# Optimization experiments

Hardware: AMD Instinct MI355X
Metric: run time of the kernel (lower is better)

Reference implementation:

```python
import jax, jax.numpy as jnp
import numpy as np


def _pick(key, nodes, mask, cnt):
    # Uniformly pick one of the `cnt` entries of `nodes` where mask is True.
    r = jax.random.randint(key, (), 0, jnp.maximum(cnt, 1))
    cs = jnp.cumsum(mask.astype(jnp.int32))
    return nodes[jnp.argmax(cs == r + 1)]


def _one_walk(key, nbrs, f0, n_faces, L):
    # nbrs: [N,3] int32 neighbor table, f0: scalar start face.
    seq = jnp.zeros((L + 1,), jnp.int32).at[0].set(f0)
    visited = jnp.zeros((n_faces + 1,), bool).at[n_faces].set(True).at[f0].set(True)

    def cond(st):
        return st[2] <= L

    def body(st):
        seq, visited, i, bs, k = st
        k, k1, k2, k3 = jax.random.split(k, 4)
        cur = seq[i - 1]
        nb = nbrs[cur]                     # [3] neighbor candidates
        unv = ~visited[nb]
        cnt = unv.sum()
        need = cnt == 0                    # stuck -> backtrack
        cand = _pick(k1, nb, unv, cnt)

        def bcond(c):
            bs_c, found = c[0], c[1]
            return need & (~found) & (i > bs_c)

        def bbody(c):
            bs_c, found, ta, kk = c
            kk, kp = jax.random.split(kk)
            back = seq[i - bs_c - 1]
            bn = nbrs[back]
            bm = ~visited[bn]
            bc = bm.sum()
            f2 = bc > 0
            ta2 = _pick(kp, bn, bm, bc)
            return (jnp.where(f2, bs_c, bs_c + 2), f2, jnp.where(f2, ta2, ta), kk)

        bs_f, found, ta_bt, _ = jax.lax.while_loop(
            bcond, bbody, (bs, jnp.array(False), jnp.int32(0), k2))
        rand_node = jax.random.randint(k3, (), 0, n_faces, dtype=jnp.int32)
        to_add = jnp.where(~need, cand, jnp.where(found, ta_bt, rand_node))
        hit = need & found                 # successful backtrack
        bs_new = jnp.where(hit, bs_f, jnp.int32(1))
        i_new = jnp.where(hit, i - bs_f, i)
        ar = jnp.arange(L + 1, dtype=jnp.int32)
        # torch: replace seq[i-bs:i] with to_add on successful backtrack
        seq = jnp.where(hit & (ar >= i_new) & (ar < i), to_add, seq)
        visited = visited.at[to_add].set(True)
        seq = seq.at[i_new].set(to_add)
        return (seq, visited, i_new + 1, bs_new, k)

    seq, *_ = jax.lax.while_loop(
        cond, body, (seq, visited, jnp.int32(1), jnp.int32(1), key))
    return seq


def patch_random_walk(key, neighbors, centers, n_faces, seq_len):
    B, G = centers.shape
    keys = jax.random.split(key, B * G).reshape(B, G)
    walk_g = jax.vmap(_one_walk, in_axes=(0, None, 0, None, None))
    walk_bg = jax.vmap(walk_g, in_axes=(0, 0, 0, None, None))
    return walk_bg(keys, neighbors, centers, n_faces, seq_len)  # [B,G,L+1] int32


def setup_inputs() -> dict:
    key = jax.random.key(0)
    k1, k2, k3 = jax.random.split(key, 3)
    B, N, G = 4, 20000, 1024
    xyz = jax.random.normal(k1, (B, N, 3), dtype=jnp.float32)
    neighbors = jax.random.randint(k2, (B, N, 3), 0, N, dtype=jnp.int32)
    centers = jax.random.randint(k3, (B, G), 0, N, dtype=jnp.int32)
    return {"xyz": xyz, "neighbors": neighbors, "centers": centers,
            "n_faces": N, "seq_len": 63}


def reference(xyz, neighbors, centers, n_faces, seq_len):
    # patch_random_walk -> idx [B,G,K]; then Group.forward gather + recenter.
    idx = patch_random_walk(jax.random.key(42), neighbors, centers, n_faces, seq_len)
    gather = jax.vmap(lambda p, i: p[i])(xyz, idx)            # [B,G,K,3]
    center_xyz = jax.vmap(lambda p, c: p[c])(xyz, centers)    # [B,G,3]
    return gather - center_xyz[:, :, None, :]
```

## Files before the change

kernel.cpp:

```cpp
#include <hip/hip_runtime.h>
#include <stdint.h>
#include <stddef.h>


namespace {

__device__ __forceinline__ uint32_t rotl32(uint32_t x, int r) {
  return (x << r) | (x >> (32 - r));
}

__device__ __forceinline__ void tf2x32(uint32_t ka, uint32_t kb,
                                       uint32_t x0, uint32_t x1,
                                       uint32_t& o0, uint32_t& o1) {
  const uint32_t kc = ka ^ kb ^ 0x1BD11BDAu;
  x0 += ka; x1 += kb;
#define TF_R4(r0, r1, r2, r3)                          \
  x0 += x1; x1 = rotl32(x1, r0); x1 ^= x0;             \
  x0 += x1; x1 = rotl32(x1, r1); x1 ^= x0;             \
  x0 += x1; x1 = rotl32(x1, r2); x1 ^= x0;             \
  x0 += x1; x1 = rotl32(x1, r3); x1 ^= x0;
  TF_R4(13, 15, 26, 6)  x0 += kb; x1 += kc + 1u;
  TF_R4(17, 29, 16, 24) x0 += kc; x1 += ka + 2u;
  TF_R4(13, 15, 26, 6)  x0 += ka; x1 += kb + 3u;
  TF_R4(17, 29, 16, 24) x0 += kb; x1 += kc + 4u;
  TF_R4(13, 15, 26, 6)  x0 += kc; x1 += ka + 5u;
#undef TF_R4
  o0 = x0; o1 = x1;
}

__device__ __forceinline__ void randbits(uint32_t ka, uint32_t kb,
                                         uint32_t& hi, uint32_t& lo) {
  uint32_t s0a, s0b, s1a, s1b, h0, h1;
  tf2x32(ka, kb, 0u, 0u, s0a, s0b);
  tf2x32(ka, kb, 0u, 1u, s1a, s1b);
  tf2x32(s0a, s0b, 0u, 0u, h0, h1);
  hi = h0 ^ h1;
  tf2x32(s1a, s1b, 0u, 0u, h0, h1);
  lo = h0 ^ h1;
}

__device__ __forceinline__ uint32_t r_generic(uint32_t hi, uint32_t lo,
                                              uint32_t span) {
  uint32_t mult = 65536u % span;
  mult = (mult * mult) % span;
  return ((hi % span) * mult + (lo % span)) % span;
}

__device__ __forceinline__ uint32_t pick_code(uint32_t hi, uint32_t lo) {
  return ((hi % 3u + lo % 3u) % 3u) | ((lo & 1u) << 2);
}

constexpr int WPB = 16;
constexpr int CH = 64;
constexpr int NMAX = 20352;
constexpr int VISW = 636;

__global__ __launch_bounds__(1024) void walk_kernel(
    const float* __restrict__ xyz, const int* __restrict__ nbrs,
    const int* __restrict__ centers, const int* __restrict__ n_faces_p,
    const int* __restrict__ seq_len_p, float* __restrict__ out,
    int s0, int num_walks, int Lp1) {
  __shared__ uint32_t nb01L[NMAX];
  __shared__ uint16_t nb2L[NMAX];
  __shared__ uint32_t visL[WPB * VISW];

  const int tid = threadIdx.x;
  const int wv = tid >> 6, lane = tid & 63;
  const int w0 = blockIdx.x * WPB;
  if (w0 >= num_walks) return;
  const int w = w0 + wv;
  const bool active = (w < num_walks);

  const int N = *n_faces_p;
  const int L = *seq_len_p;
  const int B = s0 / (3 * N);
  const int G = num_walks / B;
  const bool lds_ok = (N <= NMAX) && (G % WPB == 0);

  const int bb = (active ? w : w0) / G;
  const int* __restrict__ nb   = nbrs + (size_t)bb * N * 3;
  const float* __restrict__ xb = xyz + (size_t)bb * N * 3;

  const int f0 = active ? centers[w] : 0;
  int3 grow = make_int3(0, 0, 0);
  if (!lds_ok && active)
    grow = *reinterpret_cast<const int3*>(nb + 3 * (size_t)f0);

  if (wv == 0) {
    if (lane < WPB && (w0 + lane) < num_walks) {
      uint32_t ka, kb;
      tf2x32(0u, 42u, 0u, (uint32_t)(w0 + lane), ka, kb);
      visL[(lane * CH + 0) * 2 + 0] = ka;
      visL[(lane * CH + 0) * 2 + 1] = kb;
#pragma clang loop unroll(disable)
      for (int c2 = 1; c2 < CH; ++c2) {
        tf2x32(ka, kb, 0u, 0u, ka, kb);
        visL[(lane * CH + c2) * 2 + 0] = ka;
        visL[(lane * CH + c2) * 2 + 1] = kb;
      }
    }
  } else if (lds_ok) {
    for (int r = tid - 64; r < N; r += 960) {
      const int3 v = *reinterpret_cast<const int3*>(nb + 3 * (size_t)r);
      nb01L[r] = (uint32_t)v.x | ((uint32_t)v.y << 16);
      nb2L[r]  = (uint16_t)v.z;
    }
  }
  __syncthreads();

  const uint32_t mka = visL[(wv * CH + lane) * 2 + 0];
  const uint32_t mkb = visL[(wv * CH + lane) * 2 + 1];
  uint32_t mycode;
  {
    uint32_t k1a, k1b, hi, lo;
    tf2x32(mka, mkb, 0u, 1u, k1a, k1b);
    randbits(k1a, k1b, hi, lo);
    mycode = pick_code(hi, lo);
  }
  __syncthreads();

  if (!active) return;

  uint32_t extka = 0, extkb = 0;
  int extc = -1;
  auto get_key = [&](int idx, uint32_t& ra, uint32_t& rb) {
    if (idx < CH) {
      ra = (uint32_t)__shfl((int)mka, idx);
      rb = (uint32_t)__shfl((int)mkb, idx);
    } else {
      if (extc < 0) {
        extka = (uint32_t)__shfl((int)mka, CH - 1);
        extkb = (uint32_t)__shfl((int)mkb, CH - 1);
        extc = CH - 1;
      }
      while (extc < idx) { tf2x32(extka, extkb, 0u, 0u, extka, extkb); ++extc; }
      ra = extka; rb = extkb;
    }
  };

  int seqr = (lane == 0) ? f0 : -1;
  uint32_t code_next = (uint32_t)__shfl((int)mycode, 0);
  int i = 1, bs = 1, c = 0;

  if (lds_ok) {
    uint32_t* __restrict__ visW = visL + wv * VISW;
    for (int j = lane; j < VISW; j += 64) visW[j] = 0u;
    if (lane == 0) visW[(unsigned)f0 >> 5] = 1u << (f0 & 31);

    uint32_t p0 = nb01L[f0];
    int n0 = (int)(p0 & 0xffffu), n1 = (int)(p0 >> 16), n2 = (int)nb2L[f0];

    while (i <= L) {
      const int idx = c; ++c;
      const uint32_t pA = nb01L[n0]; const uint32_t a2 = nb2L[n0];
      const uint32_t pB = nb01L[n1]; const uint32_t b2 = nb2L[n1];
      const uint32_t pC = nb01L[n2]; const uint32_t c2v = nb2L[n2];
      const uint32_t wv0 = visW[(unsigned)n0 >> 5];
      const uint32_t wv1 = visW[(unsigned)n1 >> 5];
      const uint32_t wv2 = visW[(unsigned)n2 >> 5];
      const uint32_t codeP = code_next;
      code_next = (uint32_t)__shfl((int)mycode, (c < CH) ? c : 0);

      const uint32_t u0 = ((wv0 >> (n0 & 31)) & 1u) ^ 1u;
      const uint32_t u1 = ((wv1 >> (n1 & 31)) & 1u) ^ 1u;
      const uint32_t u2 = ((wv2 >> (n2 & 31)) & 1u) ^ 1u;
      const uint32_t cnt = u0 + u1 + u2;

      int to_add, sel;
      if (__builtin_expect(cnt == 0, 0)) {
        sel = -1;
        uint32_t kia, kib;
        get_key(idx, kia, kib);
        uint32_t kka, kkb;
        tf2x32(kia, kib, 0u, 2u, kka, kkb);
        bool found = false;
        int ta = 0, bsc = bs;
        while (!found && i > bsc) {
          uint32_t ca, cb, kpa, kpb;
          tf2x32(kka, kkb, 0u, 0u, ca, cb);
          tf2x32(kka, kkb, 0u, 1u, kpa, kpb);
          const int back = __shfl(seqr, i - bsc - 1);
          const uint32_t pm = nb01L[back];
          const int m0 = (int)(pm & 0xffffu), m1 = (int)(pm >> 16);
          const int m2 = (int)nb2L[back];
          const uint32_t e0 = ((visW[(unsigned)m0 >> 5] >> (m0 & 31)) & 1u) ^ 1u;
          const uint32_t e1 = ((visW[(unsigned)m1 >> 5] >> (m1 & 31)) & 1u) ^ 1u;
          const uint32_t e2 = ((visW[(unsigned)m2 >> 5] >> (m2 & 31)) & 1u) ^ 1u;
          const uint32_t bc = e0 + e1 + e2;
          if (bc > 0) {
            uint32_t bhi, blo;
            randbits(kpa, kpb, bhi, blo);
            const uint32_t bcode = pick_code(bhi, blo);
            const uint32_t r3 = bcode & 3u, r2 = (bcode >> 2) & 1u;
            const uint32_t t2v = (bc == 3 ? r3 : (bc == 2 ? r2 : 0)) + 1;
            ta = (e0 == t2v) ? m0 : ((e0 + e1 == t2v) ? m1 : m2);
            found = true;
          } else {
            bsc += 2;
          }
          kka = ca; kkb = cb;
        }
        if (found) {
          to_add = ta;
          const int i_new = i - bsc;
          seqr = (lane >= i_new && lane < i) ? to_add : seqr;
          bs = bsc; i = i_new;
        } else {
          uint32_t k3a, k3b, rhi, rlo;
          tf2x32(kia, kib, 0u, 3u, k3a, k3b);
          randbits(k3a, k3b, rhi, rlo);
          to_add = (int)r_generic(rhi, rlo, (uint32_t)N);
          bs = 1;
        }
        if (lane == 0)
          visW[(unsigned)to_add >> 5] |= 1u << (to_add & 31);
        seqr = (lane == i) ? to_add : seqr;
        ++i;
        const uint32_t p = nb01L[to_add];
        n0 = (int)(p & 0xffffu); n1 = (int)(p >> 16); n2 = (int)nb2L[to_add];
        continue;
      }
      uint32_t code = codeP;
      if (__builtin_expect(idx >= CH, 0)) {
        uint32_t ia, ib, k1a, k1b, hi, lo;
        get_key(idx, ia, ib);
        tf2x32(ia, ib, 0u, 1u, k1a, k1b);
        randbits(k1a, k1b, hi, lo);
        code = pick_code(hi, lo);
      }
      const uint32_t r3 = code & 3u, r2 = (code >> 2) & 1u;
      const uint32_t target = (cnt == 3 ? r3 : (cnt == 2 ? r2 : 0)) + 1;
      sel = (u0 == target) ? 0 : ((u0 + u1 == target) ? 1 : 2);
      to_add = (sel == 0) ? n0 : ((sel == 1) ? n1 : n2);
      const uint32_t wsel = (sel == 0) ? wv0 : ((sel == 1) ? wv1 : wv2);
      if (lane == 0)
        visW[(unsigned)to_add >> 5] = wsel | (1u << (to_add & 31));
      seqr = (lane == i) ? to_add : seqr;
      bs = 1; ++i;
      if (sel == 0)      { n0 = (int)(pA & 0xffffu); n1 = (int)(pA >> 16); n2 = (int)a2; }
      else if (sel == 1) { n0 = (int)(pB & 0xffffu); n1 = (int)(pB >> 16); n2 = (int)b2; }
      else               { n0 = (int)(pC & 0xffffu); n1 = (int)(pC >> 16); n2 = (int)c2v; }
    }
  } else {
    int hist  = (lane == 0) ? f0 : -1;
    int hist2 = -1;
    int3 row = grow;
    while (i <= L) {
      const int idx = c; ++c;
      const bool deep = (idx >= CH);
      const uint32_t codeP = code_next;
      code_next = (uint32_t)__shfl((int)mycode, (c < CH) ? c : 0);

      const int n0 = row.x, n1 = row.y, n2 = row.z;
      int v0 = __any(hist == n0), v1 = __any(hist == n1), v2 = __any(hist == n2);
      if (deep) {
        v0 |= __any(hist2 == n0); v1 |= __any(hist2 == n1); v2 |= __any(hist2 == n2);
      }
      const int u0 = 1 - v0, u1 = 1 - v1, u2 = 1 - v2;
      const int cnt = u0 + u1 + u2;

      int to_add;
      bool hit = false;
      int bsf = bs;
      if (cnt > 0) {
        uint32_t code = codeP;
        if (deep) {
          uint32_t ia, ib, k1a, k1b, hi, lo;
          get_key(idx, ia, ib);
          tf2x32(ia, ib, 0u, 1u, k1a, k1b);
          randbits(k1a, k1b, hi, lo);
          code = pick_code(hi, lo);
        }
        const int r3 = (int)(code & 3u), r2 = (int)((code >> 2) & 1u);
        const int target = (cnt == 3 ? r3 : (cnt == 2 ? r2 : 0)) + 1;
        to_add = (u0 == target) ? n0 : ((u0 + u1 == target) ? n1 : n2);
      } else {
        uint32_t kia, kib;
        get_key(idx, kia, kib);
        uint32_t kka, kkb;
        tf2x32(kia, kib, 0u, 2u, kka, kkb);
        bool found = false;
        int ta = 0, bsc = bs;
        while (!found && i > bsc) {
          uint32_t ca, cb, kpa, kpb;
          tf2x32(kka, kkb, 0u, 0u, ca, cb);
          tf2x32(kka, kkb, 0u, 1u, kpa, kpb);
          const int back = __shfl(seqr, i - bsc - 1);
          const int3 br = *reinterpret_cast<const int3*>(nb + 3 * (size_t)back);
          int w0m = __any(hist == br.x), w1m = __any(hist == br.y), w2m = __any(hist == br.z);
          if (deep) {
            w0m |= __any(hist2 == br.x); w1m |= __any(hist2 == br.y); w2m |= __any(hist2 == br.z);
          }
          const int e0 = 1 - w0m, e1 = 1 - w1m, e2 = 1 - w2m;
          const int bc = e0 + e1 + e2;
          if (bc > 0) {
            uint32_t bhi, blo;
            randbits(kpa, kpb, bhi, blo);
            const uint32_t bcode = pick_code(bhi, blo);
            const int r3 = (int)(bcode & 3u), r2 = (int)((bcode >> 2) & 1u);
            const int t2v = (bc == 3 ? r3 : (bc == 2 ? r2 : 0)) + 1;
            ta = (e0 == t2v) ? br.x : ((e0 + e1 == t2v) ? br.y : br.z);
            found = true;
          } else {
            bsc += 2;
          }
          kka = ca; kkb = cb;
        }
        if (found) {
          to_add = ta; hit = true; bsf = bsc;
        } else {
          uint32_t k3a, k3b, rhi, rlo;
          tf2x32(kia, kib, 0u, 3u, k3a, k3b);
          randbits(k3a, k3b, rhi, rlo);
          to_add = (int)r_generic(rhi, rlo, (uint32_t)N);
        }
      }

      int i_new, up;
      if (hit) { i_new = i - bsf; bs = bsf; up = i - 1; }
      else     { i_new = i;       bs = 1;   up = i; }
      seqr = (lane >= i_new && lane <= up) ? to_add : seqr;

      const int slot = idx + 1;
      if (slot < CH)          hist  = (lane == slot)      ? to_add : hist;
      else if (slot < 2 * CH) hist2 = (lane == slot - CH) ? to_add : hist2;

      i = i_new + 1;
      row = *reinterpret_cast<const int3*>(nb + 3 * (size_t)to_add);
    }
  }

  const float cx = xb[3 * (size_t)f0 + 0];
  const float cy = xb[3 * (size_t)f0 + 1];
  const float cz = xb[3 * (size_t)f0 + 2];
  if (lane < Lp1) {
    const int node = seqr;
    float3 v;
    v.x = xb[3 * (size_t)node + 0] - cx;
    v.y = xb[3 * (size_t)node + 1] - cy;
    v.z = xb[3 * (size_t)node + 2] - cz;
    *reinterpret_cast<float3*>(out + ((size_t)w * Lp1 + lane) * 3) = v;
  }
}

}

extern "C" void kernel_launch(void* const* d_in, const int* in_sizes, int n_in,
                              void* d_out, int out_size, void* d_ws, size_t ws_size,
                              hipStream_t stream) {
  const float* xyz     = (const float*)d_in[0];
  const int*   nbrs    = (const int*)d_in[1];
  const int*   centers = (const int*)d_in[2];
  const int*   n_faces = (const int*)d_in[3];
  const int*   seq_len = (const int*)d_in[4];
  float* out = (float*)d_out;

  const int s0 = in_sizes[0];
  const int num_walks = in_sizes[2];
  const int Lp1 = out_size / (3 * num_walks);

  const int blocks = (num_walks + WPB - 1) / WPB;
  walk_kernel<<<blocks, WPB * 64, 0, stream>>>(
      xyz, nbrs, centers, n_faces, seq_len, out, s0, num_walks, Lp1);
}
```

Baseline: 99.70 us.

## Drop LDS neighbor-table staging; prefetch neighbor rows from global memory

```diff
diff --git a/kernel.cpp b/kernel.cpp
--- a/kernel.cpp
+++ b/kernel.cpp
@@ -52,17 +52,16 @@
 
 constexpr int WPB = 16;
 constexpr int CH = 64;
-constexpr int NMAX = 20352;
-constexpr int VISW = 636;
+constexpr int KSTRIDE = 65;
+constexpr int VISW = 2048;
 
 __global__ __launch_bounds__(1024) void walk_kernel(
     const float* __restrict__ xyz, const int* __restrict__ nbrs,
     const int* __restrict__ centers, const int* __restrict__ n_faces_p,
     const int* __restrict__ seq_len_p, float* __restrict__ out,
     int s0, int num_walks, int Lp1) {
-  __shared__ uint32_t nb01L[NMAX];
-  __shared__ uint16_t nb2L[NMAX];
   __shared__ uint32_t visL[WPB * VISW];
+  __shared__ uint2 keysL[WPB * KSTRIDE];
 
   const int tid = threadIdx.x;
   const int wv = tid >> 6, lane = tid & 63;
@@ -75,41 +74,41 @@
   const int L = *seq_len_p;
   const int B = s0 / (3 * N);
   const int G = num_walks / B;
-  const bool lds_ok = (N <= NMAX) && (G % WPB == 0);
+  const bool bm_ok = (N <= VISW * 32);
 
   const int bb = (active ? w : w0) / G;
   const int* __restrict__ nb   = nbrs + (size_t)bb * N * 3;
   const float* __restrict__ xb = xyz + (size_t)bb * N * 3;
 
   const int f0 = active ? centers[w] : 0;
-  int3 grow = make_int3(0, 0, 0);
-  if (!lds_ok && active)
-    grow = *reinterpret_cast<const int3*>(nb + 3 * (size_t)f0);
-
-  if (wv == 0) {
-    if (lane < WPB && (w0 + lane) < num_walks) {
-      uint32_t ka, kb;
-      tf2x32(0u, 42u, 0u, (uint32_t)(w0 + lane), ka, kb);
-      visL[(lane * CH + 0) * 2 + 0] = ka;
-      visL[(lane * CH + 0) * 2 + 1] = kb;
+  int3 row = *reinterpret_cast<const int3*>(nb + 3 * (size_t)f0);
+
+  uint32_t* __restrict__ visW = visL + wv * VISW;
+  if (bm_ok) {
+    for (int j = lane; j < VISW; j += 64) visW[j] = 0u;
+    if (lane == 0 && active) visW[(unsigned)f0 >> 5] = 1u << (f0 & 31);
+  }
+
+  int3 t0 = *reinterpret_cast<const int3*>(nb + 3 * (size_t)row.x);
+  int3 t1 = *reinterpret_cast<const int3*>(nb + 3 * (size_t)row.y);
+  int3 t2 = *reinterpret_cast<const int3*>(nb + 3 * (size_t)row.z);
+
+  if (wv == 0 && lane < WPB && (w0 + lane) < num_walks) {
+    uint32_t ka, kb;
+    tf2x32(0u, 42u, 0u, (uint32_t)(w0 + lane), ka, kb);
+    keysL[lane * KSTRIDE + 0] = make_uint2(ka, kb);
 #pragma clang loop unroll(disable)
-      for (int c2 = 1; c2 < CH; ++c2) {
-        tf2x32(ka, kb, 0u, 0u, ka, kb);
-        visL[(lane * CH + c2) * 2 + 0] = ka;
-        visL[(lane * CH + c2) * 2 + 1] = kb;
-      }
+    for (int c2 = 1; c2 < CH; ++c2) {
+      tf2x32(ka, kb, 0u, 0u, ka, kb);
+      keysL[lane * KSTRIDE + c2] = make_uint2(ka, kb);
     }
-  } else if (lds_ok) {
-    for (int r = tid - 64; r < N; r += 960) {
-      const int3 v = *reinterpret_cast<const int3*>(nb + 3 * (size_t)r);
-      nb01L[r] = (uint32_t)v.x | ((uint32_t)v.y << 16);
-      nb2L[r]  = (uint16_t)v.z;
-    }
   }
   __syncthreads();
 
-  const uint32_t mka = visL[(wv * CH + lane) * 2 + 0];
-  const uint32_t mkb = visL[(wv * CH + lane) * 2 + 1];
+  if (!active) return;
+
+  const uint2 mykey = keysL[wv * KSTRIDE + lane];
+  const uint32_t mka = mykey.x, mkb = mykey.y;
   uint32_t mycode;
   {
     uint32_t k1a, k1b, hi, lo;
@@ -117,9 +116,6 @@
     randbits(k1a, k1b, hi, lo);
     mycode = pick_code(hi, lo);
   }
-  __syncthreads();
-
-  if (!active) return;
 
   uint32_t extka = 0, extkb = 0;
   int extc = -1;
@@ -139,28 +135,15 @@
   };
 
   int seqr = (lane == 0) ? f0 : -1;
-  uint32_t code_next = (uint32_t)__shfl((int)mycode, 0);
   int i = 1, bs = 1, c = 0;
 
-  if (lds_ok) {
-    uint32_t* __restrict__ visW = visL + wv * VISW;
-    for (int j = lane; j < VISW; j += 64) visW[j] = 0u;
-    if (lane == 0) visW[(unsigned)f0 >> 5] = 1u << (f0 & 31);
-
-    uint32_t p0 = nb01L[f0];
-    int n0 = (int)(p0 & 0xffffu), n1 = (int)(p0 >> 16), n2 = (int)nb2L[f0];
-
+  if (bm_ok) {
     while (i <= L) {
       const int idx = c; ++c;
-      const uint32_t pA = nb01L[n0]; const uint32_t a2 = nb2L[n0];
-      const uint32_t pB = nb01L[n1]; const uint32_t b2 = nb2L[n1];
-      const uint32_t pC = nb01L[n2]; const uint32_t c2v = nb2L[n2];
+      const int n0 = row.x, n1 = row.y, n2 = row.z;
       const uint32_t wv0 = visW[(unsigned)n0 >> 5];
       const uint32_t wv1 = visW[(unsigned)n1 >> 5];
       const uint32_t wv2 = visW[(unsigned)n2 >> 5];
-      const uint32_t codeP = code_next;
-      code_next = (uint32_t)__shfl((int)mycode, (c < CH) ? c : 0);
-
       const uint32_t u0 = ((wv0 >> (n0 & 31)) & 1u) ^ 1u;
       const uint32_t u1 = ((wv1 >> (n1 & 31)) & 1u) ^ 1u;
       const uint32_t u2 = ((wv2 >> (n2 & 31)) & 1u) ^ 1u;
@@ -180,12 +163,10 @@
           tf2x32(kka, kkb, 0u, 0u, ca, cb);
           tf2x32(kka, kkb, 0u, 1u, kpa, kpb);
           const int back = __shfl(seqr, i - bsc - 1);
-          const uint32_t pm = nb01L[back];
-          const int m0 = (int)(pm & 0xffffu), m1 = (int)(pm >> 16);
-          const int m2 = (int)nb2L[back];
-          const uint32_t e0 = ((visW[(unsigned)m0 >> 5] >> (m0 & 31)) & 1u) ^ 1u;
-          const uint32_t e1 = ((visW[(unsigned)m1 >> 5] >> (m1 & 31)) & 1u) ^ 1u;
-          const uint32_t e2 = ((visW[(unsigned)m2 >> 5] >> (m2 & 31)) & 1u) ^ 1u;
+          const int3 br = *reinterpret_cast<const int3*>(nb + 3 * (size_t)back);
+          const uint32_t e0 = ((visW[(unsigned)br.x >> 5] >> (br.x & 31)) & 1u) ^ 1u;
+          const uint32_t e1 = ((visW[(unsigned)br.y >> 5] >> (br.y & 31)) & 1u) ^ 1u;
+          const uint32_t e2 = ((visW[(unsigned)br.z >> 5] >> (br.z & 31)) & 1u) ^ 1u;
           const uint32_t bc = e0 + e1 + e2;
           if (bc > 0) {
             uint32_t bhi, blo;
@@ -193,7 +174,7 @@
             const uint32_t bcode = pick_code(bhi, blo);
             const uint32_t r3 = bcode & 3u, r2 = (bcode >> 2) & 1u;
             const uint32_t t2v = (bc == 3 ? r3 : (bc == 2 ? r2 : 0)) + 1;
-            ta = (e0 == t2v) ? m0 : ((e0 + e1 == t2v) ? m1 : m2);
+            ta = (e0 == t2v) ? br.x : ((e0 + e1 == t2v) ? br.y : br.z);
             found = true;
           } else {
             bsc += 2;
@@ -216,41 +197,39 @@
           visW[(unsigned)to_add >> 5] |= 1u << (to_add & 31);
         seqr = (lane == i) ? to_add : seqr;
         ++i;
-        const uint32_t p = nb01L[to_add];
-        n0 = (int)(p & 0xffffu); n1 = (int)(p >> 16); n2 = (int)nb2L[to_add];
-        continue;
+        row = *reinterpret_cast<const int3*>(nb + 3 * (size_t)to_add);
+      } else {
+        uint32_t code;
+        if (__builtin_expect(idx >= CH, 0)) {
+          uint32_t ia, ib, k1a, k1b, hi, lo;
+          get_key(idx, ia, ib);
+          tf2x32(ia, ib, 0u, 1u, k1a, k1b);
+          randbits(k1a, k1b, hi, lo);
+          code = pick_code(hi, lo);
+        } else {
+          code = (uint32_t)__builtin_amdgcn_readlane((int)mycode, idx);
+        }
+        const uint32_t r3 = code & 3u, r2 = (code >> 2) & 1u;
+        const uint32_t target = (cnt == 3 ? r3 : (cnt == 2 ? r2 : 0)) + 1;
+        sel = (u0 == target) ? 0 : ((u0 + u1 == target) ? 1 : 2);
+        to_add = (sel == 0) ? n0 : ((sel == 1) ? n1 : n2);
+        const uint32_t wsel = (sel == 0) ? wv0 : ((sel == 1) ? wv1 : wv2);
+        if (lane == 0)
+          visW[(unsigned)to_add >> 5] = wsel | (1u << (to_add & 31));
+        seqr = (lane == i) ? to_add : seqr;
+        bs = 1; ++i;
+        row = (sel == 0) ? t0 : ((sel == 1) ? t1 : t2);
       }
-      uint32_t code = codeP;
-      if (__builtin_expect(idx >= CH, 0)) {
-        uint32_t ia, ib, k1a, k1b, hi, lo;
-        get_key(idx, ia, ib);
-        tf2x32(ia, ib, 0u, 1u, k1a, k1b);
-        randbits(k1a, k1b, hi, lo);
-        code = pick_code(hi, lo);
-      }
-      const uint32_t r3 = code & 3u, r2 = (code >> 2) & 1u;
-      const uint32_t target = (cnt == 3 ? r3 : (cnt == 2 ? r2 : 0)) + 1;
-      sel = (u0 == target) ? 0 : ((u0 + u1 == target) ? 1 : 2);
-      to_add = (sel == 0) ? n0 : ((sel == 1) ? n1 : n2);
-      const uint32_t wsel = (sel == 0) ? wv0 : ((sel == 1) ? wv1 : wv2);
-      if (lane == 0)
-        visW[(unsigned)to_add >> 5] = wsel | (1u << (to_add & 31));
-      seqr = (lane == i) ? to_add : seqr;
-      bs = 1; ++i;
-      if (sel == 0)      { n0 = (int)(pA & 0xffffu); n1 = (int)(pA >> 16); n2 = (int)a2; }
-      else if (sel == 1) { n0 = (int)(pB & 0xffffu); n1 = (int)(pB >> 16); n2 = (int)b2; }
-      else               { n0 = (int)(pC & 0xffffu); n1 = (int)(pC >> 16); n2 = (int)c2v; }
+      t0 = *reinterpret_cast<const int3*>(nb + 3 * (size_t)row.x);
+      t1 = *reinterpret_cast<const int3*>(nb + 3 * (size_t)row.y);
+      t2 = *reinterpret_cast<const int3*>(nb + 3 * (size_t)row.z);
     }
   } else {
     int hist  = (lane == 0) ? f0 : -1;
     int hist2 = -1;
-    int3 row = grow;
     while (i <= L) {
       const int idx = c; ++c;
       const bool deep = (idx >= CH);
-      const uint32_t codeP = code_next;
-      code_next = (uint32_t)__shfl((int)mycode, (c < CH) ? c : 0);
-
       const int n0 = row.x, n1 = row.y, n2 = row.z;
       int v0 = __any(hist == n0), v1 = __any(hist == n1), v2 = __any(hist == n2);
       if (deep) {
@@ -263,13 +242,15 @@
       bool hit = false;
       int bsf = bs;
       if (cnt > 0) {
-        uint32_t code = codeP;
+        uint32_t code;
         if (deep) {
           uint32_t ia, ib, k1a, k1b, hi, lo;
           get_key(idx, ia, ib);
           tf2x32(ia, ib, 0u, 1u, k1a, k1b);
           randbits(k1a, k1b, hi, lo);
           code = pick_code(hi, lo);
+        } else {
+          code = (uint32_t)__builtin_amdgcn_readlane((int)mycode, idx);
         }
         const int r3 = (int)(code & 3u), r2 = (int)((code >> 2) & 1u);
         const int target = (cnt == 3 ? r3 : (cnt == 2 ? r2 : 0)) + 1;
```

Result: slower. 105.3 us (+5.6%).
